# Performance work log

Measured on AMD Instinct MI355X. Metric: run time of the kernel, lower is better.

## Reference

```python
import jax, jax.numpy as jnp
import numpy as np

PRED_LEN = 12
A = 128          # agents in the single scene
NHEAD = 8
NLAYERS = 2
D = 256          # embedding_dim
MLP = 1024
HDIM = 128       # decoder_h_dim
OBS_LEN = 8
MEMLEN = A * OBS_LEN
NEG = -1e9       # stands in for float('-inf') in the AR mask


def _sinusoid(length, d):
    pos = jnp.arange(length, dtype=jnp.float32)[:, None]
    div = jnp.exp(jnp.arange(0, d, 2, dtype=jnp.float32) * (-np.log(10000.0) / d))
    ang = pos * div
    pe = jnp.zeros((length, d), jnp.float32)
    pe = pe.at[:, 0::2].set(jnp.sin(ang))
    pe = pe.at[:, 1::2].set(jnp.cos(ang))
    return pe


def _ln(x, g, b):
    m = x.mean(-1, keepdims=True)
    v = ((x - m) ** 2).mean(-1, keepdims=True)
    return (x - m) / jnp.sqrt(v + 1e-5) * g + b


def _mha(q, k, v, Wq, bq, Wk, bk, Wv, bv, Wo, bo, mask):
    dh = D // NHEAD
    qh = (q @ Wq.T + bq).reshape(-1, NHEAD, dh)
    kh = (k @ Wk.T + bk).reshape(-1, NHEAD, dh)
    vh = (v @ Wv.T + bv).reshape(-1, NHEAD, dh)
    s = jnp.einsum('ihd,jhd->hij', qh, kh) / np.sqrt(dh) + mask[None]
    w = jax.nn.softmax(s, axis=-1)
    o = jnp.einsum('hij,jhd->ihd', w, vh).reshape(-1, D)
    return o @ Wo.T + bo


def _forward(last_pos, decoder_state, memory, agent_mask, in_W, in_b, out_W, out_b,
             sa_Wq, sa_bq, sa_Wk, sa_bk, sa_Wv, sa_bv, sa_Wo, sa_bo,
             ca_Wq, ca_bq, ca_Wk, ca_bk, ca_Wv, ca_bv, ca_Wo, ca_bo,
             ff_W1, ff_b1, ff_W2, ff_b2,
             ln1_g, ln1_b, ln2_g, ln2_b, ln3_g, ln3_b):
    agent_pe = _sinusoid(A, D)
    scene_pos = last_pos
    tokens = []
    outs = []
    for s in range(PRED_LEN):  # fixed-length AR loop (unrolled, static shapes)
        feat = jnp.concatenate([scene_pos, decoder_state], axis=-1)  # [A, 2+HDIM]
        tokens.append(feat @ in_W.T + in_b)                          # [A, D]
        steps = s + 1
        tgt = jnp.concatenate(tokens, axis=0)                        # [steps*A, D]
        time_enc = jnp.repeat(_sinusoid(steps, D), A, axis=0)
        x = tgt + time_enc + jnp.tile(agent_pe, (steps, 1))
        times = jnp.repeat(jnp.arange(steps), A)
        # generate_ar_mask: block-causal over time, tiled agent_mask within block
        tgt_mask = jnp.where(times[None, :] > times[:, None], NEG,
                             jnp.tile(agent_mask, (steps, steps)))
        # generate_mask: tiled agent_mask for cross-attention to memory
        mem_mask = jnp.tile(agent_mask, (steps, MEMLEN // A))
        for l in range(NLAYERS):
            sa = _mha(x, x, x, sa_Wq[l], sa_bq[l], sa_Wk[l], sa_bk[l],
                      sa_Wv[l], sa_bv[l], sa_Wo[l], sa_bo[l], tgt_mask)
            x = _ln(x + sa, ln1_g[l], ln1_b[l])
            ca = _mha(x, memory, memory, ca_Wq[l], ca_bq[l], ca_Wk[l], ca_bk[l],
                      ca_Wv[l], ca_bv[l], ca_Wo[l], ca_bo[l], mem_mask)
            x = _ln(x + ca, ln2_g[l], ln2_b[l])
            ff = jax.nn.relu(x @ ff_W1[l].T + ff_b1[l]) @ ff_W2[l].T + ff_b2[l]
            x = _ln(x + ff, ln3_g[l], ln3_b[l])
        rel = x[-A:] @ out_W.T + out_b                               # [A, 2]
        outs.append(rel)
        scene_pos = scene_pos + rel
    return jnp.stack(outs, axis=0)                                   # [PRED_LEN, A, 2]


def setup_inputs():
    key = jax.random.key(0)
    ks = jax.random.split(key, 40)
    def rn(k, shape, scale=0.02):
        return jax.random.normal(k, shape, jnp.float32) * scale
    inp = {
        'last_pos': jax.random.normal(ks[0], (A, 2), jnp.float32),
        'decoder_state': jax.random.normal(ks[1], (A, HDIM), jnp.float32),
        'memory': jax.random.normal(ks[2], (MEMLEN, D), jnp.float32),
        'agent_mask': jnp.zeros((A, A), jnp.float32),
        'in_W': rn(ks[3], (D, 2 + HDIM)),
        'in_b': jnp.zeros((D,), jnp.float32),
        'out_W': rn(ks[4], (2, D)),
        'out_b': jnp.zeros((2,), jnp.float32),
    }
    names = ['sa_Wq', 'sa_Wk', 'sa_Wv', 'sa_Wo', 'ca_Wq', 'ca_Wk', 'ca_Wv', 'ca_Wo']
    for i, n in enumerate(names):
        inp[n] = rn(ks[5 + i], (NLAYERS, D, D))
        inp[n.replace('W', 'b')] = jnp.zeros((NLAYERS, D), jnp.float32)
    inp['ff_W1'] = rn(ks[20], (NLAYERS, MLP, D))
    inp['ff_b1'] = jnp.zeros((NLAYERS, MLP), jnp.float32)
    inp['ff_W2'] = rn(ks[21], (NLAYERS, D, MLP))
    inp['ff_b2'] = jnp.zeros((NLAYERS, D), jnp.float32)
    for n in ['ln1', 'ln2', 'ln3']:
        inp[n + '_g'] = jnp.ones((NLAYERS, D), jnp.float32)
        inp[n + '_b'] = jnp.zeros((NLAYERS, D), jnp.float32)
    return inp


def reference(last_pos, decoder_state, memory, agent_mask, in_W, in_b, out_W, out_b,
              sa_Wq, sa_bq, sa_Wk, sa_bk, sa_Wv, sa_bv, sa_Wo, sa_bo,
              ca_Wq, ca_bq, ca_Wk, ca_bk, ca_Wv, ca_bv, ca_Wo, ca_bo,
              ff_W1, ff_b1, ff_W2, ff_b2,
              ln1_g, ln1_b, ln2_g, ln2_b, ln3_g, ln3_b):
    return _forward(last_pos, decoder_state, memory, agent_mask, in_W, in_b, out_W, out_b,
                    sa_Wq, sa_bq, sa_Wk, sa_bk, sa_Wv, sa_bv, sa_Wo, sa_bo,
                    ca_Wq, ca_bq, ca_Wk, ca_bk, ca_Wv, ca_bv, ca_Wo, ca_bo,
                    ff_W1, ff_b1, ff_W2, ff_b2,
                    ln1_g, ln1_b, ln2_g, ln2_b, ln3_g, ln3_b)
```

## Files before the change

kernel.cpp:

```cpp
#include <hip/hip_runtime.h>
#include <math.h>

#define AGENTS 128
#define DIM 256
#define NHEADS 8
#define MEM_LEN 1024
#define MLP_DIM 1024
#define PRED 12
#define MAXS (PRED * AGENTS)

typedef __attribute__((ext_vector_type(8))) short short8;
typedef __attribute__((ext_vector_type(4))) float f32x4;

#define MFMA(a, b, c) __builtin_amdgcn_mfma_f32_16x16x32_bf16(a, b, c, 0, 0, 0)

__device__ __forceinline__ unsigned short f2bf(float f) {
  union { float f; unsigned u; } v; v.f = f;
  unsigned r = v.u + 0x7fffu + ((v.u >> 16) & 1u);
  return (unsigned short)(r >> 16);
}
__device__ __forceinline__ float bf2f(unsigned short s) {
  union { unsigned u; float f; } v; v.u = (unsigned)s << 16;
  return v.f;
}

__device__ __forceinline__ short8 afrag8(const float* p) {
  float4 a = *(const float4*)p;
  float4 b = *(const float4*)(p + 4);
  short8 r;
  r[0] = (short)f2bf(a.x); r[1] = (short)f2bf(a.y);
  r[2] = (short)f2bf(a.z); r[3] = (short)f2bf(a.w);
  r[4] = (short)f2bf(b.x); r[5] = (short)f2bf(b.y);
  r[6] = (short)f2bf(b.z); r[7] = (short)f2bf(b.w);
  return r;
}

__device__ __forceinline__ void ln16(float (*sx)[264], const float* __restrict__ g,
                                     const float* __restrict__ b, int w, int l,
                                     float* __restrict__ gout, int row0)
{
#pragma unroll
  for (int rr = 0; rr < 4; ++rr) {
    int row = w * 4 + rr;
    float4 v = *(const float4*)&sx[row][l * 4];
    float s = v.x + v.y + v.z + v.w;
#pragma unroll
    for (int o = 32; o > 0; o >>= 1) s += __shfl_xor(s, o, 64);
    float mean = s * (1.0f / 256.0f);
    float dx = v.x - mean, dy = v.y - mean, dz = v.z - mean, dw = v.w - mean;
    float s2 = dx * dx + dy * dy + dz * dz + dw * dw;
#pragma unroll
    for (int o = 32; o > 0; o >>= 1) s2 += __shfl_xor(s2, o, 64);
    float rstd = rsqrtf(s2 * (1.0f / 256.0f) + 1e-5f);
    float4 gg = *(const float4*)&g[l * 4];
    float4 bb = *(const float4*)&b[l * 4];
    float4 o4 = make_float4(dx * rstd * gg.x + bb.x, dy * rstd * gg.y + bb.y,
                            dz * rstd * gg.z + bb.z, dw * rstd * gg.w + bb.w);
    *(float4*)&sx[row][l * 4] = o4;
    if (gout) *(float4*)&gout[(row0 + row) * DIM + l * 4] = o4;
  }
}

__device__ __forceinline__ void proj_row(
    const short8 afr[8], const unsigned short* __restrict__ W,
    const float* __restrict__ b, float* __restrict__ o, int row0, int w, int l)
{
  const int c15 = l & 15, r0 = (l >> 4) * 4;
  const int kl8 = (l >> 4) * 8;
  f32x4 acc[4] = {};
  const unsigned short* wp = W + (w * 64 + c15) * 256 + kl8;
#pragma unroll
  for (int kc = 0; kc < 8; ++kc)
#pragma unroll
    for (int t = 0; t < 4; ++t)
      acc[t] = MFMA(afr[kc], *(const short8*)(wp + t * 16 * 256 + kc * 32), acc[t]);
#pragma unroll
  for (int t = 0; t < 4; ++t) {
    int c = w * 64 + t * 16 + c15;
    float bb = b[c];
#pragma unroll
    for (int r = 0; r < 4; ++r)
      o[(row0 + r0 + r) * DIM + c] = acc[t][r] + bb;
  }
}

__device__ __forceinline__ void projKV(
    const short8 afr[8],
    const unsigned short* __restrict__ Wk, const float* __restrict__ bk,
    unsigned short* __restrict__ Ko,
    const unsigned short* __restrict__ Wv, const float* __restrict__ bv,
    unsigned short* __restrict__ Vo,
    int Spad, int crow, int w, int l)
{
  const int c15 = l & 15, r0 = (l >> 4) * 4;
  const int kl8 = (l >> 4) * 8;
  f32x4 acck[4] = {}, accv[4] = {};
  const unsigned short* wpk = Wk + (w * 64 + c15) * 256 + kl8;
  const unsigned short* wpv = Wv + (w * 64 + c15) * 256 + kl8;
#pragma unroll
  for (int kc = 0; kc < 8; ++kc)
#pragma unroll
    for (int t = 0; t < 4; ++t) {
      acck[t] = MFMA(afr[kc], *(const short8*)(wpk + t * 16 * 256 + kc * 32), acck[t]);
      accv[t] = MFMA(afr[kc], *(const short8*)(wpv + t * 16 * 256 + kc * 32), accv[t]);
    }
#pragma unroll
  for (int t = 0; t < 4; ++t) {
    int c = w * 64 + t * 16 + c15;
    int h = c >> 5, d = c & 31;
    float bbk = bk[c], bbv = bv[c];
#pragma unroll
    for (int r = 0; r < 4; ++r) {
      int row = crow + r0 + r;
      Ko[h * Spad * 32 + row * 32 + d] = f2bf(acck[t][r] + bbk);
      Vo[c * Spad + row] = f2bf(accv[t][r] + bbv);
    }
  }
}

__global__ __launch_bounds__(256) void embed_k(
    const float* __restrict__ scene, const float* __restrict__ ds,
    const unsigned short* __restrict__ inWb, const float* __restrict__ inb,
    const float* __restrict__ peA, const float* __restrict__ peT,
    float* __restrict__ x, int step,
    const unsigned short* __restrict__ Wq, const float* __restrict__ bq, float* __restrict__ qout,
    const unsigned short* __restrict__ Wk, const float* __restrict__ bk, unsigned short* __restrict__ kout,
    const unsigned short* __restrict__ Wv, const float* __restrict__ bv, unsigned short* __restrict__ vout,
    int cbase)
{
  __shared__ float sx[16][264];
  const int tid = threadIdx.x, l = tid & 63, w = tid >> 6;
  const int c15 = l & 15, kl8 = (l >> 4) * 8, r0 = (l >> 4) * 4;
  const int row0 = blockIdx.x * 16;
  const int mrow = row0 + c15;
  f32x4 acc[4] = {};
  for (int k0 = 0; k0 < 160; k0 += 32) {
    short8 af;
#pragma unroll
    for (int j = 0; j < 8; ++j) {
      int kk = k0 + kl8 + j;
      float v = (kk < 2) ? scene[mrow * 2 + kk]
                         : ((kk < 130) ? ds[mrow * 128 + (kk - 2)] : 0.f);
      af[j] = (short)f2bf(v);
    }
    const unsigned short* wp = inWb + (w * 64 + c15) * 160 + k0 + kl8;
#pragma unroll
    for (int t = 0; t < 4; ++t)
      acc[t] = MFMA(af, *(const short8*)(wp + t * 16 * 160), acc[t]);
  }
#pragma unroll
  for (int t = 0; t < 4; ++t) {
    int c = w * 64 + t * 16 + c15;
    float bb = inb[c] + peT[step * DIM + c];
#pragma unroll
    for (int r = 0; r < 4; ++r) {
      int row = row0 + r0 + r;
      float v = acc[t][r] + bb + peA[row * DIM + c];
      sx[r0 + r][c] = v;
      x[row * DIM + c] = v;
    }
  }
  __syncthreads();
  short8 afr[8];
#pragma unroll
  for (int kc = 0; kc < 8; ++kc) afr[kc] = afrag8(&sx[c15][kc * 32 + kl8]);
  proj_row(afr, Wq, bq, qout, row0, w, l);
  projKV(afr, Wk, bk, kout, Wv, bv, vout, MAXS, cbase + row0, w, l);
}

__global__ __launch_bounds__(256) void attn_k(
    const float* __restrict__ Q, const unsigned short* __restrict__ Kc,
    const unsigned short* __restrict__ Vt, const float* __restrict__ mask,
    float* __restrict__ O, int S, int Spad)
{
  __shared__ unsigned short pQ[4][16][80];
  const int tid = threadIdx.x, w = tid >> 6, l = tid & 63;
  const int qg = l & 15, g = l >> 4;
  const int h = blockIdx.y;
  const int qi = blockIdx.x * 64 + w * 16 + qg;

  short8 qf = afrag8(Q + qi * DIM + h * 32 + g * 8);

  float mk[2][4][4];
#pragma unroll
  for (int p = 0; p < 2; ++p)
#pragma unroll
    for (int t = 0; t < 4; ++t)
#pragma unroll
      for (int r = 0; r < 4; ++r)
        mk[p][t][r] = mask[qi * AGENTS + p * 64 + t * 16 + g * 4 + r];

  const unsigned short* kh = Kc + h * Spad * 32;
  const unsigned short* vh = Vt + h * 32 * Spad;
  unsigned short* pq = &pQ[w][0][0];
  const float scale = 0.17677669529663687f;
  f32x4 oa0 = {}, oa1 = {};
  float lsum = 0.f;

  for (int kc = 0; kc < S; kc += 64) {
    const int p = (kc >> 6) & 1;
#pragma unroll
    for (int t = 0; t < 4; ++t) {
      short8 kf = *(const short8*)(kh + (kc + t * 16 + qg) * 32 + g * 8);
      f32x4 zz = {};
      f32x4 sc = MFMA(kf, qf, zz);
      unsigned pk0, pk1;
      {
        float e0 = __expf(sc[0] * scale + mk[p][t][0]);
        float e1 = __expf(sc[1] * scale + mk[p][t][1]);
        float e2 = __expf(sc[2] * scale + mk[p][t][2]);
        float e3 = __expf(sc[3] * scale + mk[p][t][3]);
        unsigned short b0 = f2bf(e0), b1 = f2bf(e1), b2 = f2bf(e2), b3 = f2bf(e3);
        lsum += bf2f(b0) + bf2f(b1) + bf2f(b2) + bf2f(b3);
        pk0 = (unsigned)b0 | ((unsigned)b1 << 16);
        pk1 = (unsigned)b2 | ((unsigned)b3 << 16);
      }
      uint2 u2; u2.x = pk0; u2.y = pk1;
      *(uint2*)&pq[qg * 80 + t * 16 + g * 4] = u2;
    }
#pragma unroll
    for (int ks = 0; ks < 2; ++ks) {
      short8 pf = *(const short8*)&pq[qg * 80 + ks * 32 + g * 8];
      short8 v0 = *(const short8*)(vh + (0 * 16 + qg) * Spad + kc + ks * 32 + g * 8);
      short8 v1 = *(const short8*)(vh + (1 * 16 + qg) * Spad + kc + ks * 32 + g * 8);
      oa0 = MFMA(v0, pf, oa0);
      oa1 = MFMA(v1, pf, oa1);
    }
  }
  lsum += __shfl_xor(lsum, 16, 64);
  lsum += __shfl_xor(lsum, 32, 64);
  const float inv = 1.0f / lsum;
#pragma unroll
  for (int r = 0; r < 4; ++r) {
    O[qi * DIM + h * 32 + g * 4 + r] = oa0[r] * inv;
    O[qi * DIM + h * 32 + 16 + g * 4 + r] = oa1[r] * inv;
  }
}

__global__ __launch_bounds__(256) void oln_k(
    const float* __restrict__ Ain, const unsigned short* __restrict__ Wo,
    const float* __restrict__ bo, const float* __restrict__ resid,
    const float* __restrict__ g, const float* __restrict__ bv,
    float* __restrict__ xout,
    const unsigned short* __restrict__ Wq, const float* __restrict__ bq,
    float* __restrict__ qout)
{
  __shared__ float sx[16][264];
  const int tid = threadIdx.x, l = tid & 63, w = tid >> 6;
  const int c15 = l & 15, kl8 = (l >> 4) * 8, r0 = (l >> 4) * 4;
  const int row0 = blockIdx.x * 16;
  f32x4 acc[4] = {};
  const float* arow = Ain + (row0 + c15) * 256 + kl8;
  const unsigned short* wp = Wo + (w * 64 + c15) * 256 + kl8;
  for (int k0 = 0; k0 < 256; k0 += 32) {
    short8 af = afrag8(arow + k0);
#pragma unroll
    for (int t = 0; t < 4; ++t)
      acc[t] = MFMA(af, *(const short8*)(wp + t * 16 * 256 + k0), acc[t]);
  }
#pragma unroll
  for (int t = 0; t < 4; ++t) {
    int c = w * 64 + t * 16 + c15;
    float bb = bo[c];
#pragma unroll
    for (int r = 0; r < 4; ++r)
      sx[r0 + r][c] = acc[t][r] + bb + resid[(row0 + r0 + r) * DIM + c];
  }
  __syncthreads();
  ln16(sx, g, bv, w, l, xout, row0);
  __syncthreads();
  short8 afr[8];
#pragma unroll
  for (int kc = 0; kc < 8; ++kc) afr[kc] = afrag8(&sx[c15][kc * 32 + kl8]);
  proj_row(afr, Wq, bq, qout, row0, w, l);
}

template <bool QKV, bool OUTP>
__global__ __launch_bounds__(256) void ffn_k(
    const float* __restrict__ Ain, const unsigned short* __restrict__ Wo,
    const float* __restrict__ bo, const float* __restrict__ resid,
    const float* __restrict__ g2, const float* __restrict__ b2v,
    const unsigned short* __restrict__ W1, const float* __restrict__ b1v,
    const unsigned short* __restrict__ W2, const float* __restrict__ b2f,
    const float* __restrict__ g3, const float* __restrict__ b3v,
    float* __restrict__ xout,
    const unsigned short* __restrict__ Wq, const float* __restrict__ bq, float* __restrict__ qout,
    const unsigned short* __restrict__ Wk, const float* __restrict__ bk, unsigned short* __restrict__ kout,
    const unsigned short* __restrict__ Wv, const float* __restrict__ bv, unsigned short* __restrict__ vout,
    int cbase,
    const float* __restrict__ outW, const float* __restrict__ outB,
    float* __restrict__ outbuf, float* __restrict__ scene, int step)
{
  __shared__ float sx[16][264];
  __shared__ unsigned short smid[16][1032];
  const int tid = threadIdx.x, l = tid & 63, w = tid >> 6;
  const int c15 = l & 15, kl8 = (l >> 4) * 8, r0 = (l >> 4) * 4;
  const int row0 = blockIdx.x * 16;

  {
    f32x4 acc[4] = {};
    const float* arow = Ain + (row0 + c15) * 256 + kl8;
    const unsigned short* wp = Wo + (w * 64 + c15) * 256 + kl8;
    for (int k0 = 0; k0 < 256; k0 += 32) {
      short8 af = afrag8(arow + k0);
#pragma unroll
      for (int t = 0; t < 4; ++t)
        acc[t] = MFMA(af, *(const short8*)(wp + t * 16 * 256 + k0), acc[t]);
    }
#pragma unroll
    for (int t = 0; t < 4; ++t) {
      int c = w * 64 + t * 16 + c15;
      float bb = bo[c];
#pragma unroll
      for (int r = 0; r < 4; ++r)
        sx[r0 + r][c] = acc[t][r] + bb + resid[(row0 + r0 + r) * DIM + c];
    }
  }
  __syncthreads();
  ln16(sx, g2, b2v, w, l, nullptr, row0);
  __syncthreads();
  {
    short8 afr[8];
#pragma unroll
    for (int kc = 0; kc < 8; ++kc) afr[kc] = afrag8(&sx[c15][kc * 32 + kl8]);
#pragma unroll 4
    for (int t = 0; t < 16; ++t) {
      f32x4 acc = {};
      const unsigned short* wp = W1 + (w * 256 + t * 16 + c15) * 256 + kl8;
#pragma unroll
      for (int kc = 0; kc < 8; ++kc)
        acc = MFMA(afr[kc], *(const short8*)(wp + kc * 32), acc);
      int c = w * 256 + t * 16 + c15;
      float bb = b1v[c];
#pragma unroll
      for (int r = 0; r < 4; ++r)
        smid[r0 + r][c] = f2bf(fmaxf(acc[r] + bb, 0.f));
    }
  }
  __syncthreads();
  f32x4 facc[4] = {};
  for (int kc = 0; kc < 4; ++kc) {
    short8 afr[8];
#pragma unroll
    for (int kk = 0; kk < 8; ++kk)
      afr[kk] = *(const short8*)&smid[c15][kc * 256 + kk * 32 + kl8];
    const unsigned short* wp = W2 + (w * 64 + c15) * 1024 + kc * 256 + kl8;
#pragma unroll
    for (int t = 0; t < 4; ++t)
#pragma unroll
      for (int kk = 0; kk < 8; ++kk)
        facc[t] = MFMA(afr[kk], *(const short8*)(wp + t * 16 * 1024 + kk * 32), facc[t]);
  }
#pragma unroll
  for (int t = 0; t < 4; ++t) {
    int c = w * 64 + t * 16 + c15;
    float bb = b2f[c];
#pragma unroll
    for (int r = 0; r < 4; ++r)
      sx[r0 + r][c] = facc[t][r] + bb + sx[r0 + r][c];
  }
  __syncthreads();
  ln16(sx, g3, b3v, w, l, xout, row0);
  __syncthreads();
  if (QKV) {
    short8 afr[8];
#pragma unroll
    for (int kc = 0; kc < 8; ++kc) afr[kc] = afrag8(&sx[c15][kc * 32 + kl8]);
    proj_row(afr, Wq, bq, qout, row0, w, l);
    projKV(afr, Wk, bk, kout, Wv, bv, vout, MAXS, cbase + row0, w, l);
  }
  if (OUTP) {
    int il = tid >> 4, jj = (tid >> 3) & 1, kc = tid & 7;
    float a = 0.f;
    const float* sxr = &sx[il][kc * 32];
    const float* wr = outW + jj * 256 + kc * 32;
#pragma unroll
    for (int k = 0; k < 32; ++k) a += sxr[k] * wr[k];
#pragma unroll
    for (int off = 4; off > 0; off >>= 1) a += __shfl_xor(a, off, 64);
    if (kc == 0) {
      a += outB[jj];
      int gi = row0 + il;
      outbuf[(step * AGENTS + gi) * 2 + jj] = a;
      scene[gi * 2 + jj] += a;
    }
  }
}

__global__ __launch_bounds__(256) void memkv_k(
    const float* __restrict__ mem, const unsigned short* __restrict__ dxd,
    const float* __restrict__ bk, const float* __restrict__ bvv,
    unsigned short* __restrict__ memK, unsigned short* __restrict__ memV)
{
  const int li = blockIdx.z;
  const unsigned short* Wk = dxd + 5 * 131072 + li * 65536;
  const unsigned short* Wv = dxd + 6 * 131072 + li * 65536;
  const int tid = threadIdx.x, l = tid & 63, w = tid >> 6;
  const int c15 = l & 15, kl8 = (l >> 4) * 8;
  const int row0 = blockIdx.x * 16;
  short8 afr[8];
#pragma unroll
  for (int kc = 0; kc < 8; ++kc)
    afr[kc] = afrag8(mem + (row0 + c15) * 256 + kc * 32 + kl8);
  projKV(afr, Wk, bk + li * 256, memK + li * MEM_LEN * 256,
         Wv, bvv + li * 256, memV + li * MEM_LEN * 256, MEM_LEN, row0, w, l);
}

__global__ void cvt8_k(const float* p0, const float* p1, const float* p2,
                       const float* p3, const float* p4, const float* p5,
                       const float* p6, const float* p7, unsigned short* dst)
{
  const float* s;
  switch (blockIdx.z) {
    case 0: s = p0; break; case 1: s = p1; break;
    case 2: s = p2; break; case 3: s = p3; break;
    case 4: s = p4; break; case 5: s = p5; break;
    case 6: s = p6; break; default: s = p7; break;
  }
  int i = blockIdx.x * 256 + threadIdx.x;
  dst[blockIdx.z * 131072 + i] = f2bf(s[i]);
}

__global__ void cvtff_k(const float* w1, const float* w2, unsigned short* dst)
{
  const float* s = blockIdx.z ? w2 : w1;
  int i = blockIdx.x * 256 + threadIdx.x;
  dst[blockIdx.z * 524288 + i] = f2bf(s[i]);
}

__global__ void cvtinw_k(const float* w, unsigned short* dst)
{
  int i = blockIdx.x * 256 + threadIdx.x;
  if (i >= 256 * 160) return;
  int n = i / 160, k = i - n * 160;
  dst[i] = (k < 130) ? f2bf(w[n * 130 + k]) : (unsigned short)0;
}

__global__ void pe_k(float* peA, float* peT)
{
  int i = blockIdx.x * 256 + threadIdx.x;
  if (i < 128 * 256) {
    int row = i >> 8, c = i & 255, p = c >> 1;
    float dv = expf((float)(2 * p) * (-9.210340371976184f / 256.f));
    float ang = (float)row * dv;
    peA[i] = (c & 1) ? cosf(ang) : sinf(ang);
  } else if (i < 140 * 256) {
    int j = i - 32768;
    int s = j >> 8, c = j & 255, p = c >> 1;
    float dv = expf((float)(2 * p) * (-9.210340371976184f / 256.f));
    float ang = (float)s * dv;
    peT[j] = (c & 1) ? cosf(ang) : sinf(ang);
  }
}

extern "C" void kernel_launch(void* const* d_in, const int* in_sizes, int n_in,
                              void* d_out, int out_size, void* d_ws, size_t ws_size,
                              hipStream_t stream)
{
  const float* last_pos      = (const float*)d_in[0];
  const float* decoder_state = (const float*)d_in[1];
  const float* memory        = (const float*)d_in[2];
  const float* agent_mask    = (const float*)d_in[3];
  const float* in_W  = (const float*)d_in[4];
  const float* in_b  = (const float*)d_in[5];
  const float* out_W = (const float*)d_in[6];
  const float* out_b = (const float*)d_in[7];
  const float* sa_bq = (const float*)d_in[9];
  const float* sa_bk = (const float*)d_in[11];
  const float* sa_bv = (const float*)d_in[13];
  const float* sa_bo = (const float*)d_in[15];
  const float* ca_bq = (const float*)d_in[17];
  const float* ca_bk = (const float*)d_in[19];
  const float* ca_bv = (const float*)d_in[21];
  const float* ca_bo = (const float*)d_in[23];
  const float* ff_W1 = (const float*)d_in[24];
  const float* ff_b1 = (const float*)d_in[25];
  const float* ff_W2 = (const float*)d_in[26];
  const float* ff_b2 = (const float*)d_in[27];
  const float* ln1_g = (const float*)d_in[28];
  const float* ln1_b = (const float*)d_in[29];
  const float* ln2_g = (const float*)d_in[30];
  const float* ln2_b = (const float*)d_in[31];
  const float* ln3_g = (const float*)d_in[32];
  const float* ln3_b = (const float*)d_in[33];
  float* out = (float*)d_out;

  float* ws    = (float*)d_ws;
  float* scene = ws;
  float* x     = scene + 256;
  float* qbuf  = x + 32768;
  float* abuf  = qbuf + 32768;
  float* peA   = abuf + 32768;
  float* peT   = peA + 32768;
  unsigned short* saK  = (unsigned short*)(peT + 3072);
  unsigned short* saV  = saK + 2 * MAXS * 256;
  unsigned short* memK = saV + 2 * MAXS * 256;
  unsigned short* memV = memK + 2 * MEM_LEN * 256;
  unsigned short* dxdb  = memV + 2 * MEM_LEN * 256;
  unsigned short* ffW1b = dxdb + 8 * 131072;
  unsigned short* ffW2b = ffW1b + 524288;
  unsigned short* inWb  = ffW2b + 524288;

  const dim3 blk(256);
  const dim3 agrid(2, NHEADS);

  cvt8_k<<<dim3(512, 1, 8), blk, 0, stream>>>(
      (const float*)d_in[8], (const float*)d_in[10], (const float*)d_in[12],
      (const float*)d_in[14], (const float*)d_in[16], (const float*)d_in[18],
      (const float*)d_in[20], (const float*)d_in[22], dxdb);
  cvtff_k<<<dim3(2048, 1, 2), blk, 0, stream>>>(ff_W1, ff_W2, ffW1b);
  cvtinw_k<<<160, blk, 0, stream>>>(in_W, inWb);
  pe_k<<<140, blk, 0, stream>>>(peA, peT);
  memkv_k<<<dim3(64, 1, 2), blk, 0, stream>>>(memory, dxdb, ca_bk, ca_bv, memK, memV);
  hipMemcpyAsync(scene, last_pos, 256 * sizeof(float), hipMemcpyDeviceToDevice, stream);

  for (int s = 0; s < PRED; ++s) {
    embed_k<<<8, blk, 0, stream>>>(scene, decoder_state, inWb, in_b, peA, peT, x, s,
        dxdb + 0 * 131072, sa_bq, qbuf,
        dxdb + 1 * 131072, sa_bk, saK,
        dxdb + 2 * 131072, sa_bv, saV, s * AGENTS);

    for (int l = 0; l < 2; ++l) {
      const unsigned short* saWo = dxdb + 3 * 131072 + l * 65536;
      const unsigned short* caWq = dxdb + 4 * 131072 + l * 65536;
      const unsigned short* caWo = dxdb + 7 * 131072 + l * 65536;

      attn_k<<<agrid, blk, 0, stream>>>(qbuf, saK + l * MAXS * 256,
                                        saV + l * MAXS * 256, agent_mask, abuf,
                                        (s + 1) * AGENTS, MAXS);
      oln_k<<<8, blk, 0, stream>>>(abuf, saWo, sa_bo + l * 256, x,
                                   ln1_g + l * 256, ln1_b + l * 256, x,
                                   caWq, ca_bq + l * 256, qbuf);
      attn_k<<<agrid, blk, 0, stream>>>(qbuf, memK + l * MEM_LEN * 256,
                                        memV + l * MEM_LEN * 256, agent_mask, abuf,
                                        MEM_LEN, MEM_LEN);
      if (l == 0) {
        ffn_k<true, false><<<8, blk, 0, stream>>>(
            abuf, caWo, ca_bo, x, ln2_g, ln2_b,
            ffW1b, ff_b1, ffW2b, ff_b2, ln3_g, ln3_b, x,
            dxdb + 0 * 131072 + 65536, sa_bq + 256, qbuf,
            dxdb + 1 * 131072 + 65536, sa_bk + 256, saK + MAXS * 256,
            dxdb + 2 * 131072 + 65536, sa_bv + 256, saV + MAXS * 256,
            s * AGENTS,
            nullptr, nullptr, nullptr, nullptr, 0);
      } else {
        ffn_k<false, true><<<8, blk, 0, stream>>>(
            abuf, caWo, ca_bo + 256, x, ln2_g + 256, ln2_b + 256,
            ffW1b + 262144, ff_b1 + 1024, ffW2b + 262144, ff_b2 + 256,
            ln3_g + 256, ln3_b + 256, x,
            nullptr, nullptr, nullptr,
            nullptr, nullptr, nullptr,
            nullptr, nullptr, nullptr,
            0,
            out_W, out_b, out, scene, s);
      }
    }
  }
}
```

Baseline: 2.955 ms.

## Fuse the autoregressive decoder loop into one persistent kernel with grid barriers

The roughly 100 per-step launches (embed, attention, out-proj+LN, FFN) are replaced by a single persistent 8-workgroup kernel. Stages are separated by an atomic-counter grid barrier, and each workgroup takes one head or one 16-row slice per stage. Intermediate Q and attention outputs are stored as bf16, and V is moved to a blocked layout for contiguous loads. This removes launch and inter-kernel gaps, but only 8 CUs do the work, and correctness depends on all 8 workgroups being co-resident.

```diff
diff --git a/kernel.cpp b/kernel.cpp
--- a/kernel.cpp
+++ b/kernel.cpp
@@ -3,11 +3,10 @@
 
 #define AGENTS 128
 #define DIM 256
-#define NHEADS 8
 #define MEM_LEN 1024
-#define MLP_DIM 1024
 #define PRED 12
 #define MAXS (PRED * AGENTS)
+#define NWG 8
 
 typedef __attribute__((ext_vector_type(8))) short short8;
 typedef __attribute__((ext_vector_type(4))) float f32x4;
@@ -19,11 +18,9 @@
   unsigned r = v.u + 0x7fffu + ((v.u >> 16) & 1u);
   return (unsigned short)(r >> 16);
 }
-__device__ __forceinline__ float bf2f(unsigned short s) {
-  union { unsigned u; float f; } v; v.u = (unsigned)s << 16;
-  return v.f;
-}
-
+__device__ __forceinline__ float bfval(unsigned short b) {
+  union { unsigned u; float f; } v; v.u = (unsigned)b << 16; return v.f;
+}
 __device__ __forceinline__ short8 afrag8(const float* p) {
   float4 a = *(const float4*)p;
   float4 b = *(const float4*)(p + 4);
@@ -35,10 +32,40 @@
   return r;
 }
 
-__device__ __forceinline__ void ln16(float (*sx)[264], const float* __restrict__ g,
-                                     const float* __restrict__ b, int w, int l,
-                                     float* __restrict__ gout, int row0)
-{
+struct MegaP {
+  const float *last_pos, *ds, *mask;
+  const float *in_b, *out_W, *out_b;
+  const float *sa_bq, *sa_bk, *sa_bv, *sa_bo;
+  const float *ca_bq, *ca_bo;
+  const float *ff_b1, *ff_b2;
+  const float *ln1_g, *ln1_b, *ln2_g, *ln2_b, *ln3_g, *ln3_b;
+  float *out;
+  const float *peA, *peT;
+  unsigned short *qrot, *abuf;
+  unsigned short *saK, *saV;
+  const unsigned short *memK, *memV;
+  const unsigned short *dxdb, *ffW1b, *ffW2b, *inWb;
+  unsigned *barCnt;
+};
+
+__device__ __forceinline__ void gridbar(unsigned* cnt, unsigned& tgt) {
+  __syncthreads();
+  tgt += NWG;
+  if (threadIdx.x == 0) {
+    unsigned old = __hip_atomic_fetch_add(cnt, 1u, __ATOMIC_RELEASE,
+                                          __HIP_MEMORY_SCOPE_AGENT);
+    if (old + 1u < tgt) {
+      while (__hip_atomic_load(cnt, __ATOMIC_RELAXED,
+                               __HIP_MEMORY_SCOPE_AGENT) < tgt)
+        __builtin_amdgcn_s_sleep(1);
+    }
+  }
+  __syncthreads();
+  asm volatile("" ::: "memory");
+}
+
+__device__ __forceinline__ void ln16_l(float (*sx)[264], const float* __restrict__ g,
+                                       const float* __restrict__ b, int w, int l) {
 #pragma unroll
   for (int rr = 0; rr < 4; ++rr) {
     int row = w * 4 + rr;
@@ -54,356 +81,362 @@
     float rstd = rsqrtf(s2 * (1.0f / 256.0f) + 1e-5f);
     float4 gg = *(const float4*)&g[l * 4];
     float4 bb = *(const float4*)&b[l * 4];
-    float4 o4 = make_float4(dx * rstd * gg.x + bb.x, dy * rstd * gg.y + bb.y,
-                            dz * rstd * gg.z + bb.z, dw * rstd * gg.w + bb.w);
-    *(float4*)&sx[row][l * 4] = o4;
-    if (gout) *(float4*)&gout[(row0 + row) * DIM + l * 4] = o4;
-  }
-}
-
-__device__ __forceinline__ void proj_row(
-    const short8 afr[8], const unsigned short* __restrict__ W,
-    const float* __restrict__ b, float* __restrict__ o, int row0, int w, int l)
-{
-  const int c15 = l & 15, r0 = (l >> 4) * 4;
-  const int kl8 = (l >> 4) * 8;
-  f32x4 acc[4] = {};
-  const unsigned short* wp = W + (w * 64 + c15) * 256 + kl8;
-#pragma unroll
-  for (int kc = 0; kc < 8; ++kc)
-#pragma unroll
-    for (int t = 0; t < 4; ++t)
-      acc[t] = MFMA(afr[kc], *(const short8*)(wp + t * 16 * 256 + kc * 32), acc[t]);
-#pragma unroll
-  for (int t = 0; t < 4; ++t) {
-    int c = w * 64 + t * 16 + c15;
-    float bb = b[c];
-#pragma unroll
-    for (int r = 0; r < 4; ++r)
-      o[(row0 + r0 + r) * DIM + c] = acc[t][r] + bb;
-  }
-}
-
-__device__ __forceinline__ void projKV(
-    const short8 afr[8],
-    const unsigned short* __restrict__ Wk, const float* __restrict__ bk,
-    unsigned short* __restrict__ Ko,
-    const unsigned short* __restrict__ Wv, const float* __restrict__ bv,
-    unsigned short* __restrict__ Vo,
-    int Spad, int crow, int w, int l)
-{
-  const int c15 = l & 15, r0 = (l >> 4) * 4;
-  const int kl8 = (l >> 4) * 8;
-  f32x4 acck[4] = {}, accv[4] = {};
-  const unsigned short* wpk = Wk + (w * 64 + c15) * 256 + kl8;
-  const unsigned short* wpv = Wv + (w * 64 + c15) * 256 + kl8;
-#pragma unroll
-  for (int kc = 0; kc < 8; ++kc)
+    *(float4*)&sx[row][l * 4] =
+        make_float4(dx * rstd * gg.x + bb.x, dy * rstd * gg.y + bb.y,
+                    dz * rstd * gg.z + bb.z, dw * rstd * gg.w + bb.w);
+  }
+}
+
+__device__ __forceinline__ void score_tile(short8 kf, short8 qf, const float* m4,
+                                           unsigned short* dst, float& lsum) {
+  const float scale = 0.17677669529663687f;
+  f32x4 zz = {};
+  f32x4 sc = MFMA(kf, qf, zz);
+  unsigned short b0 = f2bf(__expf(sc[0] * scale + m4[0]));
+  unsigned short b1 = f2bf(__expf(sc[1] * scale + m4[1]));
+  unsigned short b2 = f2bf(__expf(sc[2] * scale + m4[2]));
+  unsigned short b3 = f2bf(__expf(sc[3] * scale + m4[3]));
+  lsum += bfval(b0) + bfval(b1) + bfval(b2) + bfval(b3);
+  uint2 u2;
+  u2.x = (unsigned)b0 | ((unsigned)b1 << 16);
+  u2.y = (unsigned)b2 | ((unsigned)b3 << 16);
+  *(uint2*)dst = u2;
+}
+
+__device__ __forceinline__ void flash64(const unsigned short* __restrict__ kh,
+                                        const unsigned short* __restrict__ vbase,
+                                        int hcol, short8 qf, const float mk[2][4][4],
+                                        int S, unsigned short* psrow,
+                                        int c15, int g8, int g,
+                                        float& lsum, f32x4& oa0, f32x4& oa1) {
+  for (int kc = 0; kc < S; kc += 64) {
+    const int pp = (kc >> 6) & 1;
 #pragma unroll
     for (int t = 0; t < 4; ++t) {
-      acck[t] = MFMA(afr[kc], *(const short8*)(wpk + t * 16 * 256 + kc * 32), acck[t]);
-      accv[t] = MFMA(afr[kc], *(const short8*)(wpv + t * 16 * 256 + kc * 32), accv[t]);
-    }
-#pragma unroll
-  for (int t = 0; t < 4; ++t) {
-    int c = w * 64 + t * 16 + c15;
-    int h = c >> 5, d = c & 31;
-    float bbk = bk[c], bbv = bv[c];
-#pragma unroll
-    for (int r = 0; r < 4; ++r) {
-      int row = crow + r0 + r;
-      Ko[h * Spad * 32 + row * 32 + d] = f2bf(acck[t][r] + bbk);
-      Vo[c * Spad + row] = f2bf(accv[t][r] + bbv);
-    }
-  }
-}
-
-__global__ __launch_bounds__(256) void embed_k(
-    const float* __restrict__ scene, const float* __restrict__ ds,
-    const unsigned short* __restrict__ inWb, const float* __restrict__ inb,
-    const float* __restrict__ peA, const float* __restrict__ peT,
-    float* __restrict__ x, int step,
-    const unsigned short* __restrict__ Wq, const float* __restrict__ bq, float* __restrict__ qout,
-    const unsigned short* __restrict__ Wk, const float* __restrict__ bk, unsigned short* __restrict__ kout,
-    const unsigned short* __restrict__ Wv, const float* __restrict__ bv, unsigned short* __restrict__ vout,
-    int cbase)
-{
-  __shared__ float sx[16][264];
-  const int tid = threadIdx.x, l = tid & 63, w = tid >> 6;
-  const int c15 = l & 15, kl8 = (l >> 4) * 8, r0 = (l >> 4) * 4;
-  const int row0 = blockIdx.x * 16;
-  const int mrow = row0 + c15;
-  f32x4 acc[4] = {};
-  for (int k0 = 0; k0 < 160; k0 += 32) {
-    short8 af;
-#pragma unroll
-    for (int j = 0; j < 8; ++j) {
-      int kk = k0 + kl8 + j;
-      float v = (kk < 2) ? scene[mrow * 2 + kk]
-                         : ((kk < 130) ? ds[mrow * 128 + (kk - 2)] : 0.f);
-      af[j] = (short)f2bf(v);
-    }
-    const unsigned short* wp = inWb + (w * 64 + c15) * 160 + k0 + kl8;
-#pragma unroll
-    for (int t = 0; t < 4; ++t)
-      acc[t] = MFMA(af, *(const short8*)(wp + t * 16 * 160), acc[t]);
-  }
-#pragma unroll
-  for (int t = 0; t < 4; ++t) {
-    int c = w * 64 + t * 16 + c15;
-    float bb = inb[c] + peT[step * DIM + c];
-#pragma unroll
-    for (int r = 0; r < 4; ++r) {
-      int row = row0 + r0 + r;
-      float v = acc[t][r] + bb + peA[row * DIM + c];
-      sx[r0 + r][c] = v;
-      x[row * DIM + c] = v;
-    }
-  }
-  __syncthreads();
-  short8 afr[8];
-#pragma unroll
-  for (int kc = 0; kc < 8; ++kc) afr[kc] = afrag8(&sx[c15][kc * 32 + kl8]);
-  proj_row(afr, Wq, bq, qout, row0, w, l);
-  projKV(afr, Wk, bk, kout, Wv, bv, vout, MAXS, cbase + row0, w, l);
-}
-
-__global__ __launch_bounds__(256) void attn_k(
-    const float* __restrict__ Q, const unsigned short* __restrict__ Kc,
-    const unsigned short* __restrict__ Vt, const float* __restrict__ mask,
-    float* __restrict__ O, int S, int Spad)
-{
-  __shared__ unsigned short pQ[4][16][80];
-  const int tid = threadIdx.x, w = tid >> 6, l = tid & 63;
-  const int qg = l & 15, g = l >> 4;
-  const int h = blockIdx.y;
-  const int qi = blockIdx.x * 64 + w * 16 + qg;
-
-  short8 qf = afrag8(Q + qi * DIM + h * 32 + g * 8);
-
-  float mk[2][4][4];
-#pragma unroll
-  for (int p = 0; p < 2; ++p)
-#pragma unroll
-    for (int t = 0; t < 4; ++t)
-#pragma unroll
-      for (int r = 0; r < 4; ++r)
-        mk[p][t][r] = mask[qi * AGENTS + p * 64 + t * 16 + g * 4 + r];
-
-  const unsigned short* kh = Kc + h * Spad * 32;
-  const unsigned short* vh = Vt + h * 32 * Spad;
-  unsigned short* pq = &pQ[w][0][0];
-  const float scale = 0.17677669529663687f;
-  f32x4 oa0 = {}, oa1 = {};
-  float lsum = 0.f;
-
-  for (int kc = 0; kc < S; kc += 64) {
-    const int p = (kc >> 6) & 1;
-#pragma unroll
-    for (int t = 0; t < 4; ++t) {
-      short8 kf = *(const short8*)(kh + (kc + t * 16 + qg) * 32 + g * 8);
-      f32x4 zz = {};
-      f32x4 sc = MFMA(kf, qf, zz);
-      unsigned pk0, pk1;
-      {
-        float e0 = __expf(sc[0] * scale + mk[p][t][0]);
-        float e1 = __expf(sc[1] * scale + mk[p][t][1]);
-        float e2 = __expf(sc[2] * scale + mk[p][t][2]);
-        float e3 = __expf(sc[3] * scale + mk[p][t][3]);
-        unsigned short b0 = f2bf(e0), b1 = f2bf(e1), b2 = f2bf(e2), b3 = f2bf(e3);
-        lsum += bf2f(b0) + bf2f(b1) + bf2f(b2) + bf2f(b3);
-        pk0 = (unsigned)b0 | ((unsigned)b1 << 16);
-        pk1 = (unsigned)b2 | ((unsigned)b3 << 16);
-      }
-      uint2 u2; u2.x = pk0; u2.y = pk1;
-      *(uint2*)&pq[qg * 80 + t * 16 + g * 4] = u2;
+      short8 kf = *(const short8*)(kh + (kc + t * 16 + c15) * 32 + g8);
+      score_tile(kf, qf, mk[pp][t], psrow + t * 16 + g * 4, lsum);
     }
 #pragma unroll
     for (int ks = 0; ks < 2; ++ks) {
-      short8 pf = *(const short8*)&pq[qg * 80 + ks * 32 + g * 8];
-      short8 v0 = *(const short8*)(vh + (0 * 16 + qg) * Spad + kc + ks * 32 + g * 8);
-      short8 v1 = *(const short8*)(vh + (1 * 16 + qg) * Spad + kc + ks * 32 + g * 8);
+      short8 pf = *(const short8*)(psrow + ks * 32 + g8);
+      int j = kc + ks * 32 + g8;
+      const unsigned short* vb = vbase + (j >> 4) * 4096 + (j & 15);
+      short8 v0 = *(const short8*)(vb + (hcol + c15) * 16);
+      short8 v1 = *(const short8*)(vb + (hcol + c15 + 16) * 16);
       oa0 = MFMA(v0, pf, oa0);
       oa1 = MFMA(v1, pf, oa1);
     }
   }
-  lsum += __shfl_xor(lsum, 16, 64);
-  lsum += __shfl_xor(lsum, 32, 64);
-  const float inv = 1.0f / lsum;
-#pragma unroll
-  for (int r = 0; r < 4; ++r) {
-    O[qi * DIM + h * 32 + g * 4 + r] = oa0[r] * inv;
-    O[qi * DIM + h * 32 + 16 + g * 4 + r] = oa1[r] * inv;
-  }
-}
-
-__global__ __launch_bounds__(256) void oln_k(
-    const float* __restrict__ Ain, const unsigned short* __restrict__ Wo,
-    const float* __restrict__ bo, const float* __restrict__ resid,
-    const float* __restrict__ g, const float* __restrict__ bv,
-    float* __restrict__ xout,
-    const unsigned short* __restrict__ Wq, const float* __restrict__ bq,
-    float* __restrict__ qout)
-{
+}
+
+__device__ void embed_rows(const MegaP& p, float (*sx)[264], float (*sscene)[2],
+                           int wg, int s, int c15, int g8, int r0v, int w) {
+  const int rowb = wg * 16;
+  const int arow = rowb + c15;
+  f32x4 acc[4] = {};
+  const unsigned short* wp = p.inWb + (w * 64 + c15) * 160 + g8;
+  for (int kc = 0; kc < 5; ++kc) {
+    short8 af;
+#pragma unroll
+    for (int j = 0; j < 8; ++j) {
+      int kk = kc * 32 + g8 + j;
+      float v = (kk < 2) ? sscene[c15][kk]
+                         : ((kk < 130) ? p.ds[arow * 128 + (kk - 2)] : 0.f);
+      af[j] = (short)f2bf(v);
+    }
+#pragma unroll
+    for (int t = 0; t < 4; ++t)
+      acc[t] = MFMA(af, *(const short8*)(wp + t * 16 * 160 + kc * 32), acc[t]);
+  }
+#pragma unroll
+  for (int t = 0; t < 4; ++t) {
+    int col = w * 64 + t * 16 + c15;
+    float bb = p.in_b[col] + p.peT[s * DIM + col];
+#pragma unroll
+    for (int r = 0; r < 4; ++r)
+      sx[r0v + r][col] = acc[t][r] + bb + p.peA[(rowb + r0v + r) * DIM + col];
+  }
+}
+
+__device__ void qkv_rows(const MegaP& p, float (*sx)[264], int wg, int s, int li,
+                         int c15, int g8, int r0v, int w, unsigned short* qdst) {
+  const int rowb = wg * 16;
+  short8 af[8];
+#pragma unroll
+  for (int kc = 0; kc < 8; ++kc) af[kc] = afrag8(&sx[c15][kc * 32 + g8]);
+  const unsigned short* wpq = p.dxdb + 0 * 131072 + li * 65536 + (w * 64 + c15) * 256 + g8;
+  const unsigned short* wpk = p.dxdb + 1 * 131072 + li * 65536 + (w * 64 + c15) * 256 + g8;
+  const unsigned short* wpv = p.dxdb + 2 * 131072 + li * 65536 + (w * 64 + c15) * 256 + g8;
+  f32x4 aq[4] = {}, ak[4] = {}, av[4] = {};
+#pragma unroll
+  for (int kc = 0; kc < 8; ++kc) {
+#pragma unroll
+    for (int t = 0; t < 4; ++t) {
+      aq[t] = MFMA(af[kc], *(const short8*)(wpq + t * 16 * 256 + kc * 32), aq[t]);
+      ak[t] = MFMA(af[kc], *(const short8*)(wpk + t * 16 * 256 + kc * 32), ak[t]);
+      av[t] = MFMA(af[kc], *(const short8*)(wpv + t * 16 * 256 + kc * 32), av[t]);
+    }
+  }
+  unsigned short* saKl = p.saK + li * 393216;
+  unsigned short* saVl = p.saV + li * 393216;
+  const float* bq = p.sa_bq + li * 256;
+  const float* bk = p.sa_bk + li * 256;
+  const float* bv = p.sa_bv + li * 256;
+#pragma unroll
+  for (int t = 0; t < 4; ++t) {
+    int col = w * 64 + t * 16 + c15;
+    float bbq = bq[col], bbk = bk[col], bbv = bv[col];
+    int hh = col >> 5, d = col & 31;
+#pragma unroll
+    for (int r = 0; r < 4; ++r) {
+      qdst[(rowb + r0v + r) * 256 + col] = f2bf(aq[t][r] + bbq);
+      saKl[hh * (MAXS * 32) + (s * 128 + rowb + r0v + r) * 32 + d] = f2bf(ak[t][r] + bbk);
+    }
+    unsigned long long pk = 0;
+#pragma unroll
+    for (int r = 0; r < 4; ++r)
+      pk |= (unsigned long long)f2bf(av[t][r] + bbv) << (16 * r);
+    *(unsigned long long*)&saVl[((s * 8 + wg) * 256 + col) * 16 + r0v] = pk;
+  }
+}
+
+__device__ void attn_sa(const MegaP& p, unsigned short (*ps)[16][96], int wg, int s,
+                        int li, int c15, int g, int g8, int w,
+                        const unsigned short* __restrict__ qsrc,
+                        unsigned short* __restrict__ adst) {
+  const int h = wg;
+  const int S = (s + 1) * 128;
+  const unsigned short* kh = p.saK + li * 393216 + h * (MAXS * 32);
+  const unsigned short* vbase = p.saV + li * 393216;
+  for (int rb = 0; rb < 2; ++rb) {
+    const int qrow = rb * 64 + w * 16 + c15;
+    short8 qf = *(const short8*)(qsrc + qrow * 256 + h * 32 + g8);
+    float mk[2][4][4];
+#pragma unroll
+    for (int pp = 0; pp < 2; ++pp)
+#pragma unroll
+      for (int t = 0; t < 4; ++t)
+#pragma unroll
+        for (int r = 0; r < 4; ++r)
+          mk[pp][t][r] = p.mask[qrow * AGENTS + pp * 64 + t * 16 + g * 4 + r];
+    f32x4 oa0 = {}, oa1 = {};
+    float lsum = 0.f;
+    flash64(kh, vbase, h * 32, qf, mk, S, &ps[w][c15][0], c15, g8, g, lsum, oa0, oa1);
+    lsum += __shfl_xor(lsum, 16, 64);
+    lsum += __shfl_xor(lsum, 32, 64);
+    const float inv = 1.0f / lsum;
+    unsigned long long pk0 = 0, pk1 = 0;
+#pragma unroll
+    for (int r = 0; r < 4; ++r) {
+      pk0 |= (unsigned long long)f2bf(oa0[r] * inv) << (16 * r);
+      pk1 |= (unsigned long long)f2bf(oa1[r] * inv) << (16 * r);
+    }
+    *(unsigned long long*)(adst + h * 4096 + qrow * 32 + g * 4) = pk0;
+    *(unsigned long long*)(adst + h * 4096 + qrow * 32 + 16 + g * 4) = pk1;
+  }
+}
+
+__global__ __launch_bounds__(256, 1) void mega_k(MegaP p) {
   __shared__ float sx[16][264];
+  __shared__ unsigned short sca[16][264];
+  __shared__ unsigned short smid[16][1040];
+  __shared__ unsigned short squ[4][16][64];
+  __shared__ unsigned short ps[4][16][96];
+  __shared__ float sscene[16][2];
+
+  const int wg = blockIdx.x;
   const int tid = threadIdx.x, l = tid & 63, w = tid >> 6;
-  const int c15 = l & 15, kl8 = (l >> 4) * 8, r0 = (l >> 4) * 4;
-  const int row0 = blockIdx.x * 16;
-  f32x4 acc[4] = {};
-  const float* arow = Ain + (row0 + c15) * 256 + kl8;
-  const unsigned short* wp = Wo + (w * 64 + c15) * 256 + kl8;
-  for (int k0 = 0; k0 < 256; k0 += 32) {
-    short8 af = afrag8(arow + k0);
-#pragma unroll
-    for (int t = 0; t < 4; ++t)
-      acc[t] = MFMA(af, *(const short8*)(wp + t * 16 * 256 + k0), acc[t]);
-  }
-#pragma unroll
-  for (int t = 0; t < 4; ++t) {
-    int c = w * 64 + t * 16 + c15;
-    float bb = bo[c];
-#pragma unroll
-    for (int r = 0; r < 4; ++r)
-      sx[r0 + r][c] = acc[t][r] + bb + resid[(row0 + r0 + r) * DIM + c];
-  }
+  const int c15 = l & 15, g = l >> 4, g8 = g * 8, r0v = g * 4;
+  const int rowb = wg * 16;
+  unsigned tgt = 0;
+#define GB gridbar(p.barCnt, tgt)
+
+  if (tid < 32)
+    sscene[tid >> 1][tid & 1] = p.last_pos[(rowb + (tid >> 1)) * 2 + (tid & 1)];
   __syncthreads();
-  ln16(sx, g, bv, w, l, xout, row0);
+  embed_rows(p, sx, sscene, wg, 0, c15, g8, r0v, w);
   __syncthreads();
-  short8 afr[8];
-#pragma unroll
-  for (int kc = 0; kc < 8; ++kc) afr[kc] = afrag8(&sx[c15][kc * 32 + kl8]);
-  proj_row(afr, Wq, bq, qout, row0, w, l);
-}
-
-template <bool QKV, bool OUTP>
-__global__ __launch_bounds__(256) void ffn_k(
-    const float* __restrict__ Ain, const unsigned short* __restrict__ Wo,
-    const float* __restrict__ bo, const float* __restrict__ resid,
-    const float* __restrict__ g2, const float* __restrict__ b2v,
-    const unsigned short* __restrict__ W1, const float* __restrict__ b1v,
-    const unsigned short* __restrict__ W2, const float* __restrict__ b2f,
-    const float* __restrict__ g3, const float* __restrict__ b3v,
-    float* __restrict__ xout,
-    const unsigned short* __restrict__ Wq, const float* __restrict__ bq, float* __restrict__ qout,
-    const unsigned short* __restrict__ Wk, const float* __restrict__ bk, unsigned short* __restrict__ kout,
-    const unsigned short* __restrict__ Wv, const float* __restrict__ bv, unsigned short* __restrict__ vout,
-    int cbase,
-    const float* __restrict__ outW, const float* __restrict__ outB,
-    float* __restrict__ outbuf, float* __restrict__ scene, int step)
-{
-  __shared__ float sx[16][264];
-  __shared__ unsigned short smid[16][1032];
-  const int tid = threadIdx.x, l = tid & 63, w = tid >> 6;
-  const int c15 = l & 15, kl8 = (l >> 4) * 8, r0 = (l >> 4) * 4;
-  const int row0 = blockIdx.x * 16;
-
-  {
-    f32x4 acc[4] = {};
-    const float* arow = Ain + (row0 + c15) * 256 + kl8;
-    const unsigned short* wp = Wo + (w * 64 + c15) * 256 + kl8;
-    for (int k0 = 0; k0 < 256; k0 += 32) {
-      short8 af = afrag8(arow + k0);
-#pragma unroll
-      for (int t = 0; t < 4; ++t)
-        acc[t] = MFMA(af, *(const short8*)(wp + t * 16 * 256 + k0), acc[t]);
-    }
-#pragma unroll
-    for (int t = 0; t < 4; ++t) {
-      int c = w * 64 + t * 16 + c15;
-      float bb = bo[c];
-#pragma unroll
-      for (int r = 0; r < 4; ++r)
-        sx[r0 + r][c] = acc[t][r] + bb + resid[(row0 + r0 + r) * DIM + c];
-    }
-  }
-  __syncthreads();
-  ln16(sx, g2, b2v, w, l, nullptr, row0);
-  __syncthreads();
-  {
-    short8 afr[8];
-#pragma unroll
-    for (int kc = 0; kc < 8; ++kc) afr[kc] = afrag8(&sx[c15][kc * 32 + kl8]);
+  qkv_rows(p, sx, wg, 0, 0, c15, g8, r0v, w, p.qrot);
+
+  for (int s = 0; s < PRED; ++s) {
+    for (int li = 0; li < 2; ++li) {
+      const int rot = s * 2 + li;
+      GB;
+      attn_sa(p, ps, wg, s, li, c15, g, g8, w,
+              p.qrot + rot * 32768, p.abuf + rot * 32768);
+      GB;
+      {
+        const unsigned short* ab = p.abuf + rot * 32768;
+        const unsigned short* wp = p.dxdb + 3 * 131072 + li * 65536 + (w * 64 + c15) * 256 + g8;
+        f32x4 acc[4] = {};
+#pragma unroll
+        for (int kc = 0; kc < 8; ++kc) {
+          short8 af = *(const short8*)(ab + kc * 4096 + (rowb + c15) * 32 + g8);
+#pragma unroll
+          for (int t = 0; t < 4; ++t)
+            acc[t] = MFMA(af, *(const short8*)(wp + t * 16 * 256 + kc * 32), acc[t]);
+        }
+        const float* bo = p.sa_bo + li * 256;
+#pragma unroll
+        for (int t = 0; t < 4; ++t) {
+          int col = w * 64 + t * 16 + c15;
+          float bb = bo[col];
+#pragma unroll
+          for (int r = 0; r < 4; ++r) sx[r0v + r][col] += acc[t][r] + bb;
+        }
+      }
+      __syncthreads();
+      ln16_l(sx, p.ln1_g + li * 256, p.ln1_b + li * 256, w, l);
+      __syncthreads();
+      {
+        short8 af[8];
+#pragma unroll
+        for (int kc = 0; kc < 8; ++kc) af[kc] = afrag8(&sx[c15][kc * 32 + g8]);
+        const unsigned short* wp = p.dxdb + 4 * 131072 + li * 65536 + (w * 64 + c15) * 256 + g8;
+        f32x4 aq[4] = {};
+#pragma unroll
+        for (int kc = 0; kc < 8; ++kc)
+#pragma unroll
+          for (int t = 0; t < 4; ++t)
+            aq[t] = MFMA(af[kc], *(const short8*)(wp + t * 16 * 256 + kc * 32), aq[t]);
+        const float* bq = p.ca_bq + li * 256;
+#pragma unroll
+        for (int t = 0; t < 4; ++t) {
+          int col = w * 64 + t * 16 + c15;
+          float bb = bq[col];
+#pragma unroll
+          for (int r = 0; r < 4; ++r)
+            squ[w][r0v + r][t * 16 + c15] = f2bf(aq[t][r] + bb);
+        }
+      }
+      {
+        const int arow = rowb + c15;
+        float mk[2][4][4];
+#pragma unroll
+        for (int pp = 0; pp < 2; ++pp)
+#pragma unroll
+          for (int t = 0; t < 4; ++t)
+#pragma unroll
+            for (int r = 0; r < 4; ++r)
+              mk[pp][t][r] = p.mask[arow * AGENTS + pp * 64 + t * 16 + g * 4 + r];
+        const unsigned short* vbase = p.memV + li * 262144;
+#pragma unroll
+        for (int hh2 = 0; hh2 < 2; ++hh2) {
+          const int hh = w * 2 + hh2;
+          short8 qf = *(const short8*)&squ[w][c15][hh2 * 32 + g8];
+          const unsigned short* kh = p.memK + li * 262144 + hh * (MEM_LEN * 32);
+          f32x4 oa0 = {}, oa1 = {};
+          float lsum = 0.f;
+          flash64(kh, vbase, hh * 32, qf, mk, MEM_LEN, &ps[w][c15][0],
+                  c15, g8, g, lsum, oa0, oa1);
+          lsum += __shfl_xor(lsum, 16, 64);
+          lsum += __shfl_xor(lsum, 32, 64);
+          const float inv = 1.0f / lsum;
+          unsigned long long pk0 = 0, pk1 = 0;
+#pragma unroll
+          for (int r = 0; r < 4; ++r) {
+            pk0 |= (unsigned long long)f2bf(oa0[r] * inv) << (16 * r);
+            pk1 |= (unsigned long long)f2bf(oa1[r] * inv) << (16 * r);
+          }
+          *(unsigned long long*)&sca[c15][hh * 32 + g * 4] = pk0;
+          *(unsigned long long*)&sca[c15][hh * 32 + 16 + g * 4] = pk1;
+        }
+      }
+      __syncthreads();
+      {
+        const unsigned short* wp = p.dxdb + 7 * 131072 + li * 65536 + (w * 64 + c15) * 256 + g8;
+        f32x4 acc[4] = {};
+#pragma unroll
+        for (int kc = 0; kc < 8; ++kc) {
+          short8 af = *(const short8*)&sca[c15][kc * 32 + g8];
+#pragma unroll
+          for (int t = 0; t < 4; ++t)
+            acc[t] = MFMA(af, *(const short8*)(wp + t * 16 * 256 + kc * 32), acc[t]);
+        }
+        const float* bo = p.ca_bo + li * 256;
+#pragma unroll
+        for (int t = 0; t < 4; ++t) {
+          int col = w * 64 + t * 16 + c15;
+          float bb = bo[col];
+#pragma unroll
+          for (int r = 0; r < 4; ++r) sx[r0v + r][col] += acc[t][r] + bb;
+        }
+      }
+      __syncthreads();
+      ln16_l(sx, p.ln2_g + li * 256, p.ln2_b + li * 256, w, l);
+      __syncthreads();
+      {
+        short8 af[8];
+#pragma unroll
+        for (int kc = 0; kc < 8; ++kc) af[kc] = afrag8(&sx[c15][kc * 32 + g8]);
+        const unsigned short* W1 = p.ffW1b + li * 262144;
+        const float* b1 = p.ff_b1 + li * 1024;
 #pragma unroll 4
-    for (int t = 0; t < 16; ++t) {
-      f32x4 acc = {};
-      const unsigned short* wp = W1 + (w * 256 + t * 16 + c15) * 256 + kl8;
-#pragma unroll
-      for (int kc = 0; kc < 8; ++kc)
-        acc = MFMA(afr[kc], *(const short8*)(wp + kc * 32), acc);
-      int c = w * 256 + t * 16 + c15;
-      float bb = b1v[c];
-#pragma unroll
-      for (int r = 0; r < 4; ++r)
-        smid[r0 + r][c] = f2bf(fmaxf(acc[r] + bb, 0.f));
-    }
-  }
-  __syncthreads();
-  f32x4 facc[4] = {};
-  for (int kc = 0; kc < 4; ++kc) {
-    short8 afr[8];
-#pragma unroll
-    for (int kk = 0; kk < 8; ++kk)
-      afr[kk] = *(const short8*)&smid[c15][kc * 256 + kk * 32 + kl8];
-    const unsigned short* wp = W2 + (w * 64 + c15) * 1024 + kc * 256 + kl8;
-#pragma unroll
-    for (int t = 0; t < 4; ++t)
-#pragma unroll
-      for (int kk = 0; kk < 8; ++kk)
-        facc[t] = MFMA(afr[kk], *(const short8*)(wp + t * 16 * 1024 + kk * 32), facc[t]);
-  }
-#pragma unroll
-  for (int t = 0; t < 4; ++t) {
-    int c = w * 64 + t * 16 + c15;
-    float bb = b2f[c];
-#pragma unroll
-    for (int r = 0; r < 4; ++r)
-      sx[r0 + r][c] = facc[t][r] + bb + sx[r0 + r][c];
-  }
-  __syncthreads();
-  ln16(sx, g3, b3v, w, l, xout, row0);
-  __syncthreads();
-  if (QKV) {
-    short8 afr[8];
-#pragma unroll
-    for (int kc = 0; kc < 8; ++kc) afr[kc] = afrag8(&sx[c15][kc * 32 + kl8]);
-    proj_row(afr, Wq, bq, qout, row0, w, l);
-    projKV(afr, Wk, bk, kout, Wv, bv, vout, MAXS, cbase + row0, w, l);
-  }
-  if (OUTP) {
-    int il = tid >> 4, jj = (tid >> 3) & 1, kc = tid & 7;
-    float a = 0.f;
-    const float* sxr = &sx[il][kc * 32];
-    const float* wr = outW + jj * 256 + kc * 32;
-#pragma unroll
-    for (int k = 0; k < 32; ++k) a += sxr[k] * wr[k];
-#pragma unroll
-    for (int off = 4; off > 0; off >>= 1) a += __shfl_xor(a, off, 64);
-    if (kc == 0) {
-      a += outB[jj];
-      int gi = row0 + il;
-      outbuf[(step * AGENTS + gi) * 2 + jj] = a;
-      scene[gi * 2 + jj] += a;
-    }
-  }
-}
-
-__global__ __launch_bounds__(256) void memkv_k(
-    const float* __restrict__ mem, const unsigned short* __restrict__ dxd,
-    const float* __restrict__ bk, const float* __restrict__ bvv,
-    unsigned short* __restrict__ memK, unsigned short* __restrict__ memV)
-{
-  const int li = blockIdx.z;
-  const unsigned short* Wk = dxd + 5 * 131072 + li * 65536;
-  const unsigned short* Wv = dxd + 6 * 131072 + li * 65536;
-  const int tid = threadIdx.x, l = tid & 63, w = tid >> 6;
-  const int c15 = l & 15, kl8 = (l >> 4) * 8;
-  const int row0 = blockIdx.x * 16;
-  short8 afr[8];
-#pragma unroll
-  for (int kc = 0; kc < 8; ++kc)
-    afr[kc] = afrag8(mem + (row0 + c15) * 256 + kc * 32 + kl8);
-  projKV(afr, Wk, bk + li * 256, memK + li * MEM_LEN * 256,
-         Wv, bvv + li * 256, memV + li * MEM_LEN * 256, MEM_LEN, row0, w, l);
+        for (int t = 0; t < 16; ++t) {
+          f32x4 a1 = {};
+          const unsigned short* wp = W1 + (w * 256 + t * 16 + c15) * 256 + g8;
+#pragma unroll
+          for (int kc = 0; kc < 8; ++kc)
+            a1 = MFMA(af[kc], *(const short8*)(wp + kc * 32), a1);
+          int col = w * 256 + t * 16 + c15;
+          float bb = b1[col];
+#pragma unroll
+          for (int r = 0; r < 4; ++r)
+            smid[r0v + r][col] = f2bf(fmaxf(a1[r] + bb, 0.f));
+        }
+      }
+      __syncthreads();
+      {
+        const unsigned short* wp = p.ffW2b + li * 262144 + (w * 64 + c15) * 1024 + g8;
+        f32x4 acc[4] = {};
+        for (int kc = 0; kc < 32; ++kc) {
+          short8 af = *(const short8*)&smid[c15][kc * 32 + g8];
+#pragma unroll
+          for (int t = 0; t < 4; ++t)
+            acc[t] = MFMA(af, *(const short8*)(wp + t * 16 * 1024 + kc * 32), acc[t]);
+        }
+        const float* b2 = p.ff_b2 + li * 256;
+#pragma unroll
+        for (int t = 0; t < 4; ++t) {
+          int col = w * 64 + t * 16 + c15;
+          float bb = b2[col];
+#pragma unroll
+          for (int r = 0; r < 4; ++r) sx[r0v + r][col] += acc[t][r] + bb;
+        }
+      }
+      __syncthreads();
+      ln16_l(sx, p.ln3_g + li * 256, p.ln3_b + li * 256, w, l);
+      __syncthreads();
+      if (li == 0) {
+        qkv_rows(p, sx, wg, s, 1, c15, g8, r0v, w, p.qrot + (s * 2 + 1) * 32768);
+      } else {
+        {
+          int row16 = tid >> 4, j = (tid >> 3) & 1, kc2 = tid & 7;
+          float a = 0.f;
+          const float* wr = p.out_W + j * 256 + kc2 * 32;
+          const float* xr = &sx[row16][kc2 * 32];
+#pragma unroll
+          for (int k = 0; k < 32; ++k) a += xr[k] * wr[k];
+          a += __shfl_xor(a, 1, 64);
+          a += __shfl_xor(a, 2, 64);
+          a += __shfl_xor(a, 4, 64);
+          if (kc2 == 0) {
+            a += p.out_b[j];
+            p.out[(s * AGENTS + rowb + row16) * 2 + j] = a;
+            if (s < PRED - 1) sscene[row16][j] += a;
+          }
+        }
+        __syncthreads();
+        if (s < PRED - 1) {
+          embed_rows(p, sx, sscene, wg, s + 1, c15, g8, r0v, w);
+          __syncthreads();
+          qkv_rows(p, sx, wg, s + 1, 0, c15, g8, r0v, w,
+                   p.qrot + (s + 1) * 2 * 32768);
+        }
+      }
+    }
+  }
+#undef GB
 }
 
 __global__ void cvt8_k(const float* p0, const float* p1, const float* p2,
@@ -440,120 +473,119 @@
 {
   int i = blockIdx.x * 256 + threadIdx.x;
   if (i < 128 * 256) {
-    int row = i >> 8, c = i & 255, p = c >> 1;
-    float dv = expf((float)(2 * p) * (-9.210340371976184f / 256.f));
+    int row = i >> 8, c = i & 255, pp = c >> 1;
+    float dv = expf((float)(2 * pp) * (-9.210340371976184f / 256.f));
     float ang = (float)row * dv;
     peA[i] = (c & 1) ? cosf(ang) : sinf(ang);
   } else if (i < 140 * 256) {
     int j = i - 32768;
-    int s = j >> 8, c = j & 255, p = c >> 1;
-    float dv = expf((float)(2 * p) * (-9.210340371976184f / 256.f));
+    int s = j >> 8, c = j & 255, pp = c >> 1;
+    float dv = expf((float)(2 * pp) * (-9.210340371976184f / 256.f));
     float ang = (float)s * dv;
     peT[j] = (c & 1) ? cosf(ang) : sinf(ang);
   }
 }
+
+__global__ __launch_bounds__(256) void memkv_k(
+    const float* __restrict__ mem, const unsigned short* __restrict__ dxd,
+    const float* __restrict__ bk, const float* __restrict__ bvv,
+    unsigned short* __restrict__ memK, unsigned short* __restrict__ memV)
+{
+  const int li = blockIdx.z;
+  const int y = blockIdx.y;
+  const bool isK = y < 4;
+  const int colb = (y & 3) * 64;
+  const unsigned short* W = dxd + (isK ? 5 : 6) * 131072 + li * 65536;
+  const float* bias = (isK ? bk : bvv) + li * 256;
+  unsigned short* Ko = memK + li * 262144;
+  unsigned short* Vo = memV + li * 262144;
+  const int tid = threadIdx.x, l = tid & 63, w = tid >> 6;
+  const int c15 = l & 15, g8 = (l >> 4) * 8, r0v = (l >> 4) * 4;
+  const int rowb = blockIdx.x * 64 + w * 16;
+  const int arow = rowb + c15;
+  f32x4 acc[4] = {};
+  const unsigned short* wp = W + (colb + c15) * 256 + g8;
+  for (int kc = 0; kc < 8; ++kc) {
+    short8 af = afrag8(mem + arow * 256 + kc * 32 + g8);
+#pragma unroll
+    for (int t = 0; t < 4; ++t)
+      acc[t] = MFMA(af, *(const short8*)(wp + t * 16 * 256 + kc * 32), acc[t]);
+  }
+  const int kb = blockIdx.x * 4 + w;
+#pragma unroll
+  for (int t = 0; t < 4; ++t) {
+    const int col = colb + t * 16 + c15;
+    const float bb = bias[col];
+    if (isK) {
+      const int hh = col >> 5, d = col & 31;
+#pragma unroll
+      for (int r = 0; r < 4; ++r)
+        Ko[hh * (MEM_LEN * 32) + (rowb + r0v + r) * 32 + d] = f2bf(acc[t][r] + bb);
+    } else {
+      unsigned long long pk = 0;
+#pragma unroll
+      for (int r = 0; r < 4; ++r)
+        pk |= (unsigned long long)f2bf(acc[t][r] + bb) << (16 * r);
+      *(unsigned long long*)&Vo[(kb * 256 + col) * 16 + r0v] = pk;
+    }
+  }
+}
+
+__global__ void initbar_k(unsigned* b) { b[0] = 0; }
 
 extern "C" void kernel_launch(void* const* d_in, const int* in_sizes, int n_in,
                               void* d_out, int out_size, void* d_ws, size_t ws_size,
                               hipStream_t stream)
 {
-  const float* last_pos      = (const float*)d_in[0];
-  const float* decoder_state = (const float*)d_in[1];
-  const float* memory        = (const float*)d_in[2];
-  const float* agent_mask    = (const float*)d_in[3];
-  const float* in_W  = (const float*)d_in[4];
-  const float* in_b  = (const float*)d_in[5];
-  const float* out_W = (const float*)d_in[6];
-  const float* out_b = (const float*)d_in[7];
-  const float* sa_bq = (const float*)d_in[9];
-  const float* sa_bk = (const float*)d_in[11];
-  const float* sa_bv = (const float*)d_in[13];
-  const float* sa_bo = (const float*)d_in[15];
-  const float* ca_bq = (const float*)d_in[17];
-  const float* ca_bk = (const float*)d_in[19];
-  const float* ca_bv = (const float*)d_in[21];
-  const float* ca_bo = (const float*)d_in[23];
-  const float* ff_W1 = (const float*)d_in[24];
-  const float* ff_b1 = (const float*)d_in[25];
-  const float* ff_W2 = (const float*)d_in[26];
-  const float* ff_b2 = (const float*)d_in[27];
-  const float* ln1_g = (const float*)d_in[28];
-  const float* ln1_b = (const float*)d_in[29];
-  const float* ln2_g = (const float*)d_in[30];
-  const float* ln2_b = (const float*)d_in[31];
-  const float* ln3_g = (const float*)d_in[32];
-  const float* ln3_b = (const float*)d_in[33];
-  float* out = (float*)d_out;
-
-  float* ws    = (float*)d_ws;
-  float* scene = ws;
-  float* x     = scene + 256;
-  float* qbuf  = x + 32768;
-  float* abuf  = qbuf + 32768;
-  float* peA   = abuf + 32768;
-  float* peT   = peA + 32768;
-  unsigned short* saK  = (unsigned short*)(peT + 3072);
-  unsigned short* saV  = saK + 2 * MAXS * 256;
-  unsigned short* memK = saV + 2 * MAXS * 256;
-  unsigned short* memV = memK + 2 * MEM_LEN * 256;
-  unsigned short* dxdb  = memV + 2 * MEM_LEN * 256;
+  float* ws = (float*)d_ws;
+  float* peA = ws;
+  float* peT = peA + 32768;
+  unsigned short* qrot = (unsigned short*)(peT + 3072);
+  unsigned short* abuf = qrot + 24 * 32768;
+  unsigned short* saK  = abuf + 24 * 32768;
+  unsigned short* saV  = saK + 2 * 393216;
+  unsigned short* memK = saV + 2 * 393216;
+  unsigned short* memV = memK + 2 * 262144;
+  unsigned short* dxdb = memV + 2 * 262144;
   unsigned short* ffW1b = dxdb + 8 * 131072;
   unsigned short* ffW2b = ffW1b + 524288;
   unsigned short* inWb  = ffW2b + 524288;
+  unsigned* bar = (unsigned*)(inWb + 40960);
 
   const dim3 blk(256);
-  const dim3 agrid(2, NHEADS);
 
   cvt8_k<<<dim3(512, 1, 8), blk, 0, stream>>>(
       (const float*)d_in[8], (const float*)d_in[10], (const float*)d_in[12],
       (const float*)d_in[14], (const float*)d_in[16], (const float*)d_in[18],
       (const float*)d_in[20], (const float*)d_in[22], dxdb);
-  cvtff_k<<<dim3(2048, 1, 2), blk, 0, stream>>>(ff_W1, ff_W2, ffW1b);
-  cvtinw_k<<<160, blk, 0, stream>>>(in_W, inWb);
+  cvtff_k<<<dim3(2048, 1, 2), blk, 0, stream>>>((const float*)d_in[24],
+                                                (const float*)d_in[26], ffW1b);
+  cvtinw_k<<<160, blk, 0, stream>>>((const float*)d_in[4], inWb);
   pe_k<<<140, blk, 0, stream>>>(peA, peT);
-  memkv_k<<<dim3(64, 1, 2), blk, 0, stream>>>(memory, dxdb, ca_bk, ca_bv, memK, memV);
-  hipMemcpyAsync(scene, last_pos, 256 * sizeof(float), hipMemcpyDeviceToDevice, stream);
-
-  for (int s = 0; s < PRED; ++s) {
-    embed_k<<<8, blk, 0, stream>>>(scene, decoder_state, inWb, in_b, peA, peT, x, s,
-        dxdb + 0 * 131072, sa_bq, qbuf,
-        dxdb + 1 * 131072, sa_bk, saK,
-        dxdb + 2 * 131072, sa_bv, saV, s * AGENTS);
-
-    for (int l = 0; l < 2; ++l) {
-      const unsigned short* saWo = dxdb + 3 * 131072 + l * 65536;
-      const unsigned short* caWq = dxdb + 4 * 131072 + l * 65536;
-      const unsigned short* caWo = dxdb + 7 * 131072 + l * 65536;
-
-      attn_k<<<agrid, blk, 0, stream>>>(qbuf, saK + l * MAXS * 256,
-                                        saV + l * MAXS * 256, agent_mask, abuf,
-                                        (s + 1) * AGENTS, MAXS);
-      oln_k<<<8, blk, 0, stream>>>(abuf, saWo, sa_bo + l * 256, x,
-                                   ln1_g + l * 256, ln1_b + l * 256, x,
-                                   caWq, ca_bq + l * 256, qbuf);
-      attn_k<<<agrid, blk, 0, stream>>>(qbuf, memK + l * MEM_LEN * 256,
-                                        memV + l * MEM_LEN * 256, agent_mask, abuf,
-                                        MEM_LEN, MEM_LEN);
-      if (l == 0) {
-        ffn_k<true, false><<<8, blk, 0, stream>>>(
-            abuf, caWo, ca_bo, x, ln2_g, ln2_b,
-            ffW1b, ff_b1, ffW2b, ff_b2, ln3_g, ln3_b, x,
-            dxdb + 0 * 131072 + 65536, sa_bq + 256, qbuf,
-            dxdb + 1 * 131072 + 65536, sa_bk + 256, saK + MAXS * 256,
-            dxdb + 2 * 131072 + 65536, sa_bv + 256, saV + MAXS * 256,
-            s * AGENTS,
-            nullptr, nullptr, nullptr, nullptr, 0);
-      } else {
-        ffn_k<false, true><<<8, blk, 0, stream>>>(
-            abuf, caWo, ca_bo + 256, x, ln2_g + 256, ln2_b + 256,
-            ffW1b + 262144, ff_b1 + 1024, ffW2b + 262144, ff_b2 + 256,
-            ln3_g + 256, ln3_b + 256, x,
-            nullptr, nullptr, nullptr,
-            nullptr, nullptr, nullptr,
-            nullptr, nullptr, nullptr,
-            0,
-            out_W, out_b, out, scene, s);
-      }
-    }
-  }
-}
+  memkv_k<<<dim3(16, 8, 2), blk, 0, stream>>>((const float*)d_in[2], dxdb,
+      (const float*)d_in[19], (const float*)d_in[21], memK, memV);
+  initbar_k<<<1, 1, 0, stream>>>(bar);
+
+  MegaP p;
+  p.last_pos = (const float*)d_in[0];
+  p.ds = (const float*)d_in[1];
+  p.mask = (const float*)d_in[3];
+  p.in_b = (const float*)d_in[5];
+  p.out_W = (const float*)d_in[6];
+  p.out_b = (const float*)d_in[7];
+  p.sa_bq = (const float*)d_in[9];  p.sa_bk = (const float*)d_in[11];
+  p.sa_bv = (const float*)d_in[13]; p.sa_bo = (const float*)d_in[15];
+  p.ca_bq = (const float*)d_in[17]; p.ca_bo = (const float*)d_in[23];
+  p.ff_b1 = (const float*)d_in[25]; p.ff_b2 = (const float*)d_in[27];
+  p.ln1_g = (const float*)d_in[28]; p.ln1_b = (const float*)d_in[29];
+  p.ln2_g = (const float*)d_in[30]; p.ln2_b = (const float*)d_in[31];
+  p.ln3_g = (const float*)d_in[32]; p.ln3_b = (const float*)d_in[33];
+  p.out = (float*)d_out;
+  p.peA = peA; p.peT = peT;
+  p.qrot = qrot; p.abuf = abuf;
+  p.saK = saK; p.saV = saV; p.memK = memK; p.memV = memV;
+  p.dxdb = dxdb; p.ffW1b = ffW1b; p.ffW2b = ffW2b; p.inWb = inWb;
+  p.barCnt = bar;
+
+  mega_k<<<dim3(NWG), blk, 0, stream>>>(p);
+}
```

Measured after the change: 5.770 ms. +95.3%, slower.
